# Optimization experiments

Hardware: AMD Instinct MI355X
Metric: run time of the kernel (lower is better)

## Reference

```python
import jax, jax.numpy as jnp
import numpy as np

DECAY = 0.97
TEMP = 0.7
EPS = 1e-6
NORM_EPS = 1e-12  # torch F.normalize default eps


def _l2norm(x, axis=-1):
    n = jnp.linalg.norm(x, axis=axis, keepdims=True)
    return x / jnp.maximum(n, NORM_EPS)


def setup_inputs() -> dict:
    key = jax.random.key(0)
    k1, k2, k3 = jax.random.split(key, 3)
    pair_embed = jax.random.normal(k1, (8, 2048, 1024), dtype=jnp.float32)
    patterns = _l2norm(jax.random.normal(k2, (4096, 1024), dtype=jnp.float32))
    usage = jax.random.uniform(k3, (4096,), dtype=jnp.float32)
    return {"pair_embed": pair_embed, "patterns": patterns, "usage": usage}


def reference(pair_embed, patterns, usage):
    G, D = patterns.shape
    flat = pair_embed.reshape(-1, D)                      # [N, D]
    queries = _l2norm(flat)
    pat_n = _l2norm(patterns)
    logits = queries @ pat_n.T                             # [N, G]
    homeostasis = jnp.log(jnp.clip(usage, EPS))
    weights = jax.nn.softmax((logits - homeostasis[None, :]) / TEMP, axis=-1)

    # Hebbian EMA update (mirrors update(); no_grad in original)
    flat_assign = weights                                  # [N, G]
    weights_sum = flat_assign.sum(axis=0)                  # [G]
    valid = weights_sum > 0
    usage_new = usage * DECAY
    usage_new = jnp.where(valid, usage_new + (1.0 - DECAY) * weights_sum, usage_new)
    updates = flat_assign.T @ flat                         # [G, D]
    updates = updates / (weights_sum[:, None] + EPS)
    blended = _l2norm(patterns * DECAY + (1.0 - DECAY) * updates)
    patterns_new = jnp.where(valid[:, None], blended, patterns)

    out_weights = weights.reshape(*pair_embed.shape[:-1], G)
    return out_weights, patterns_new, usage_new
```

## Files before the change

### kernel.cpp

```cpp
#include <hip/hip_runtime.h>
#include <stdint.h>
#include <math.h>


#define DECAY 0.97f
#define OMD 0.03f
#define INV_TEMP (1.0f / 0.7f)
#define EPS 1e-6f
#define NORM_EPS 1e-12f

constexpr int NROWS = 16384;
constexpr int DK = 1024;
constexpr int GP = 4096;

typedef unsigned short u16;
typedef __bf16 bf16x8 __attribute__((ext_vector_type(8)));
typedef float f32x4 __attribute__((ext_vector_type(4)));

__device__ inline u16 f2bf(float x) {
    union { float f; uint32_t u; } c; c.f = x;
    uint32_t r = c.u + 0x7fffu + ((c.u >> 16) & 1u);
    return (u16)(r >> 16);
}

__device__ inline void gl_lds16(const u16* g, u16* l) {
    __builtin_amdgcn_global_load_lds(
        (const __attribute__((address_space(1))) void*)g,
        (__attribute__((address_space(3))) void*)l, 16, 0, 0);
}

__global__ __launch_bounds__(256) void norm_rows_kernel(
        const float* __restrict__ in, u16* __restrict__ outn) {
    __shared__ float sred[4];
    const int row = blockIdx.x;
    const int t = threadIdx.x;
    const float4 v = ((const float4*)(in + (size_t)row * DK))[t];
    float ss = v.x * v.x + v.y * v.y + v.z * v.z + v.w * v.w;
#pragma unroll
    for (int o = 32; o > 0; o >>= 1) ss += __shfl_xor(ss, o);
    if ((t & 63) == 0) sred[t >> 6] = ss;
    __syncthreads();
    const float tot = sred[0] + sred[1] + sred[2] + sred[3];
    const float rs = 1.0f / fmaxf(sqrtf(tot), NORM_EPS);
    ushort4 o4;
    o4.x = f2bf(v.x * rs); o4.y = f2bf(v.y * rs);
    o4.z = f2bf(v.z * rs); o4.w = f2bf(v.w * rs);
    ((ushort4*)(outn + (size_t)row * DK))[t] = o4;
}

__global__ __launch_bounds__(256) void prep_scalars_kernel(
        const float* __restrict__ usage, float* __restrict__ hscaled,
        float* __restrict__ wsum, float* __restrict__ rowsum) {
    const int i = blockIdx.x * 256 + threadIdx.x;
    if (i < GP) {
        hscaled[i] = logf(fmaxf(usage[i], EPS)) * INV_TEMP;
        wsum[i] = 0.0f;
    }
    rowsum[i] = 0.0f;
}

__global__ __launch_bounds__(256) void rowinv_kernel(float* __restrict__ rowsum) {
    const int i = blockIdx.x * 256 + threadIdx.x;
    rowsum[i] = 1.0f / rowsum[i];
}

__global__ __launch_bounds__(256) void zero_kernel(float4* __restrict__ p) {
    p[(size_t)blockIdx.x * 256 + threadIdx.x] = (float4){0.f, 0.f, 0.f, 0.f};
}

__global__ __launch_bounds__(256) void transpose_f32_bf16_kernel(
        const float* __restrict__ in, u16* __restrict__ out, int R, int C) {
    __shared__ float tile[64][260];
    const int r0 = blockIdx.x * 64;
    const int c0 = blockIdx.y * 256;
    const int t = threadIdx.x;
    const int fr = t & 63;
    const int rr = t >> 6;
#pragma unroll
    for (int j = 0; j < 16; ++j) {
        const int r = rr + 4 * j;
        const float4 v = *(const float4*)(in + (size_t)(r0 + r) * C + c0 + fr * 4);
        *(float4*)&tile[r][fr * 4] = v;
    }
    __syncthreads();
    __align__(16) u16 tmp[64];
#pragma unroll
    for (int r = 0; r < 64; ++r) tmp[r] = f2bf(tile[r][t]);
    u16* op = out + (size_t)(c0 + t) * R + r0;
#pragma unroll
    for (int i = 0; i < 8; ++i) ((uint4*)op)[i] = ((const uint4*)tmp)[i];
}

__global__ __launch_bounds__(256) void scale_transpose_kernel(
        float* __restrict__ W, const float* __restrict__ invs,
        u16* __restrict__ wT, float* __restrict__ wsum) {
    __shared__ float tile[64][260];
    __shared__ float sinv[64];
    const int r0 = blockIdx.x * 64;
    const int c0 = blockIdx.y * 256;
    const int t = threadIdx.x;
    if (t < 64) sinv[t] = invs[r0 + t];
    __syncthreads();
    const int fr = t & 63;
    const int rr = t >> 6;
#pragma unroll
    for (int j = 0; j < 16; ++j) {
        const int r = rr + 4 * j;
        float4 v = *(const float4*)(W + (size_t)(r0 + r) * GP + c0 + fr * 4);
        const float s = sinv[r];
        v.x *= s; v.y *= s; v.z *= s; v.w *= s;
        *(float4*)(W + (size_t)(r0 + r) * GP + c0 + fr * 4) = v;
        *(float4*)&tile[r][fr * 4] = v;
    }
    __syncthreads();
    __align__(16) u16 tmp[64];
    float csum = 0.f;
#pragma unroll
    for (int r = 0; r < 64; ++r) {
        const float x = tile[r][t];
        csum += x;
        tmp[r] = f2bf(x);
    }
    u16* op = wT + (size_t)(c0 + t) * NROWS + r0;
#pragma unroll
    for (int i = 0; i < 8; ++i) ((uint4*)op)[i] = ((const uint4*)tmp)[i];
    atomicAdd(&wsum[c0 + t], csum);
}

template <int KSTEPS, int KLD>
__device__ inline void gemm_bt_tile(const u16* __restrict__ A,
                                    const u16* __restrict__ B,
                                    int m0, int n0, int k0,
                                    u16* As, u16* Bs, f32x4 acc[4][4]) {
    const int t = threadIdx.x;
    const int lane = t & 63;
    const int wave = t >> 6;
    const int wm = (wave >> 1) * 64;
    const int wn = (wave & 1) * 64;
    const int fr = lane & 15;
    const int q8 = lane >> 4;

    const int srow = 32 * wave + (lane >> 3);
    const int soct = (lane & 7) ^ ((lane >> 3) & 7);
    const size_t a_base = (size_t)(m0 + srow) * KLD + k0 + soct * 8;
    const size_t b_base = (size_t)(n0 + srow) * KLD + k0 + soct * 8;

#pragma unroll 1
    for (int kt = 0; kt < KSTEPS; kt += 64) {
        __syncthreads();
#pragma unroll
        for (int i = 0; i < 4; ++i) {
            gl_lds16(A + a_base + (size_t)(8 * i) * KLD + kt,
                     As + (32 * wave + 8 * i) * 64);
            gl_lds16(B + b_base + (size_t)(8 * i) * KLD + kt,
                     Bs + (32 * wave + 8 * i) * 64);
        }
        __syncthreads();
#pragma unroll
        for (int ks8 = 0; ks8 < 8; ks8 += 4) {
            bf16x8 af[4], bfr[4];
#pragma unroll
            for (int f = 0; f < 4; ++f) {
                const int ra = wm + f * 16 + fr;
                af[f]  = *(const bf16x8*)(As + ra * 64 + (((ks8 + q8) ^ (ra & 7)) * 8));
                const int rb = wn + f * 16 + fr;
                bfr[f] = *(const bf16x8*)(Bs + rb * 64 + (((ks8 + q8) ^ (rb & 7)) * 8));
            }
#pragma unroll
            for (int fm = 0; fm < 4; ++fm)
#pragma unroll
                for (int fn = 0; fn < 4; ++fn)
                    acc[fm][fn] = __builtin_amdgcn_mfma_f32_16x16x32_bf16(
                        af[fm], bfr[fn], acc[fm][fn], 0, 0, 0);
        }
    }
}

__global__ __launch_bounds__(256) void gemm1_kernel(
        const u16* __restrict__ Q, const u16* __restrict__ P,
        const float* __restrict__ hs, float* __restrict__ Wout,
        float* __restrict__ rowsum) {
    __shared__ u16 As[128 * 64];
    __shared__ u16 Bs[128 * 64];
    const int bid0 = blockIdx.x;
    const int bid = (bid0 & 7) * 512 + (bid0 >> 3);
    const int m0 = (bid >> 5) * 128;
    const int n0 = (bid & 31) * 128;
    f32x4 acc[4][4];
#pragma unroll
    for (int a = 0; a < 4; ++a)
#pragma unroll
        for (int b = 0; b < 4; ++b) acc[a][b] = (f32x4){0.f, 0.f, 0.f, 0.f};
    gemm_bt_tile<DK, DK>(Q, P, m0, n0, 0, As, Bs, acc);

    const int lane = threadIdx.x & 63;
    const int wave = threadIdx.x >> 6;
    const int wm = (wave >> 1) * 64, wn = (wave & 1) * 64;
    const int cq = lane & 15, rq = (lane >> 4) * 4;
    float hval[4];
#pragma unroll
    for (int fn = 0; fn < 4; ++fn) hval[fn] = hs[n0 + wn + fn * 16 + cq];
#pragma unroll
    for (int fm = 0; fm < 4; ++fm) {
        const int mb = m0 + wm + fm * 16 + rq;
#pragma unroll
        for (int r = 0; r < 4; ++r) {
            float rs = 0.f;
#pragma unroll
            for (int fn = 0; fn < 4; ++fn) {
                const int g = n0 + wn + fn * 16 + cq;
                const float e = __expf(acc[fm][fn][r] * INV_TEMP - hval[fn]);
                Wout[(size_t)(mb + r) * GP + g] = e;
                rs += e;
            }
#pragma unroll
            for (int o = 1; o < 16; o <<= 1) rs += __shfl_xor(rs, o);
            if (cq == 0) atomicAdd(&rowsum[mb + r], rs);
        }
    }
}

__global__ __launch_bounds__(256) void gemm2_kernel(
        const u16* __restrict__ WT, const u16* __restrict__ FT,
        float* __restrict__ Upart) {
    __shared__ u16 As[128 * 64];
    __shared__ u16 Bs[128 * 64];
    const int bid = blockIdx.x;
    const int k0 = (bid & 7) * 2048;
    const int n0 = ((bid >> 3) & 7) * 128;
    const int m0 = (bid >> 6) * 128;
    f32x4 acc[4][4];
#pragma unroll
    for (int a = 0; a < 4; ++a)
#pragma unroll
        for (int b = 0; b < 4; ++b) acc[a][b] = (f32x4){0.f, 0.f, 0.f, 0.f};
    gemm_bt_tile<2048, NROWS>(WT, FT, m0, n0, k0, As, Bs, acc);

    const int lane = threadIdx.x & 63;
    const int wave = threadIdx.x >> 6;
    const int wm = (wave >> 1) * 64, wn = (wave & 1) * 64;
    const int cq = lane & 15, rq = (lane >> 4) * 4;
#pragma unroll
    for (int fn = 0; fn < 4; ++fn) {
        const int d = n0 + wn + fn * 16 + cq;
#pragma unroll
        for (int fm = 0; fm < 4; ++fm) {
            const int gb = m0 + wm + fm * 16 + rq;
#pragma unroll
            for (int r = 0; r < 4; ++r)
                atomicAdd(&Upart[(size_t)(gb + r) * DK + d], acc[fm][fn][r]);
        }
    }
}

__global__ __launch_bounds__(256) void usage_kernel(
        const float* __restrict__ usage, const float* __restrict__ wsum,
        float* __restrict__ Uout, float* __restrict__ invw) {
    const int g = blockIdx.x * 256 + threadIdx.x;
    if (g < GP) {
        const float s = wsum[g];
        Uout[g] = usage[g] * DECAY + (s > 0.f ? OMD * s : 0.f);
        invw[g] = 1.0f / (s + EPS);
    }
}

__global__ __launch_bounds__(256) void finalize_patterns_kernel(
        const float* __restrict__ patterns, const float* __restrict__ wsum,
        const float* __restrict__ invw, const float* __restrict__ Upart,
        float* __restrict__ Pout) {
    __shared__ float sred[4];
    const int g = blockIdx.x;
    const int t = threadIdx.x;
    const float iw = invw[g] * OMD;
    const float4 u4 = ((const float4*)(Upart + (size_t)g * DK))[t];
    const float4 p4 = ((const float4*)(patterns + (size_t)g * DK))[t];
    float4 b;
    b.x = DECAY * p4.x + iw * u4.x;
    b.y = DECAY * p4.y + iw * u4.y;
    b.z = DECAY * p4.z + iw * u4.z;
    b.w = DECAY * p4.w + iw * u4.w;
    float ss = b.x * b.x + b.y * b.y + b.z * b.z + b.w * b.w;
#pragma unroll
    for (int o = 32; o > 0; o >>= 1) ss += __shfl_xor(ss, o);
    if ((t & 63) == 0) sred[t >> 6] = ss;
    __syncthreads();
    const float tot = sred[0] + sred[1] + sred[2] + sred[3];
    const float rs = 1.0f / fmaxf(sqrtf(tot), NORM_EPS);
    float4 o4;
    if (wsum[g] > 0.f) {
        o4.x = b.x * rs; o4.y = b.y * rs; o4.z = b.z * rs; o4.w = b.w * rs;
    } else {
        o4 = p4;
    }
    ((float4*)(Pout + (size_t)g * DK))[t] = o4;
}

extern "C" void kernel_launch(void* const* d_in, const int* in_sizes, int n_in,
                              void* d_out, int out_size, void* d_ws, size_t ws_size,
                              hipStream_t stream) {
    const float* pair_embed = (const float*)d_in[0];
    const float* patterns   = (const float*)d_in[1];
    const float* usage      = (const float*)d_in[2];

    float* out_w = (float*)d_out;
    float* out_p = out_w + (size_t)NROWS * GP;
    float* out_u = out_p + (size_t)GP * DK;

    char* ws = (char*)d_ws;
    u16* q_bf   = (u16*)(ws);
    float* Upart = (float*)(ws);
    u16* pat_bf = (u16*)(ws + 33554432);
    u16* fT     = (u16*)(ws + 41943040);
    u16* wT     = (u16*)(ws + 75497472);
    float* hs   = (float*)(ws + 209715200);
    float* wsum = (float*)(ws + 209715200 + 16384);
    float* invw = (float*)(ws + 209715200 + 32768);
    float* rsum = (float*)(ws + 209715200 + 49152);

    prep_scalars_kernel<<<64, 256, 0, stream>>>(usage, hs, wsum, rsum);
    norm_rows_kernel<<<NROWS, 256, 0, stream>>>(pair_embed, q_bf);
    norm_rows_kernel<<<GP, 256, 0, stream>>>(patterns, pat_bf);
    {
        dim3 g(NROWS / 64, DK / 256);
        transpose_f32_bf16_kernel<<<g, 256, 0, stream>>>(pair_embed, fT, NROWS, DK);
    }
    gemm1_kernel<<<(NROWS / 128) * (GP / 128), 256, 0, stream>>>(q_bf, pat_bf, hs, out_w, rsum);
    rowinv_kernel<<<64, 256, 0, stream>>>(rsum);
    {
        dim3 g(NROWS / 64, GP / 256);
        scale_transpose_kernel<<<g, 256, 0, stream>>>(out_w, rsum, wT, wsum);
    }
    usage_kernel<<<16, 256, 0, stream>>>(usage, wsum, out_u, invw);
    zero_kernel<<<(GP * DK / 4) / 256, 256, 0, stream>>>((float4*)Upart);
    gemm2_kernel<<<8 * (GP / 128) * (DK / 128), 256, 0, stream>>>(wT, fT, Upart);
    finalize_patterns_kernel<<<GP, 256, 0, stream>>>(patterns, wsum, invw, Upart, out_p);
}
```

Measured before the change: 925.9 us.

## Use 256x128 tiles with 8 waves and triple-buffered LDS prefetch in GEMMs

Both GEMM kernels move from 128x128 tiles with 4 waves and a load-sync-compute loop to 256x128 tiles with 8 waves. A three-slot LDS ring prefetches two k-steps ahead using vmcnt waits and a single barrier per step. MFMA sections are raised to higher priority with setprio. The goal is to hide global-to-LDS latency and raise B-tile reuse, at the cost of about 144KB of LDS per block, which limits occupancy. The bid swizzle in gemm1 is also removed.

```diff
diff --git a/kernel.cpp b/kernel.cpp
--- a/kernel.cpp
+++ b/kernel.cpp
@@ -128,10 +128,12 @@
 }
 
 template <int KSTEPS, int KLD>
-__device__ inline void gemm_bt_tile(const u16* __restrict__ A,
-                                    const u16* __restrict__ B,
-                                    int m0, int n0, int k0,
-                                    u16* As, u16* Bs, f32x4 acc[4][4]) {
+__device__ inline void gemm_bt_256x128(const u16* __restrict__ A,
+                                       const u16* __restrict__ B,
+                                       int m0, int n0, int k0,
+                                       u16* sm, f32x4 acc[4][4]) {
+    constexpr int SLOT = 24576;
+    constexpr int BOFF = 16384;
     const int t = threadIdx.x;
     const int lane = t & 63;
     const int wave = t >> 6;
@@ -140,58 +142,85 @@
     const int fr = lane & 15;
     const int q8 = lane >> 4;
 
-    const int srow = 32 * wave + (lane >> 3);
-    const int soct = (lane & 7) ^ ((lane >> 3) & 7);
-    const size_t a_base = (size_t)(m0 + srow) * KLD + k0 + soct * 8;
-    const size_t b_base = (size_t)(n0 + srow) * KLD + k0 + soct * 8;
-
+    const int arow = 32 * wave + (lane >> 3);
+    const int brow = 16 * wave + (lane >> 3);
+    const size_t a_base = (size_t)(m0 + arow) * KLD + k0 + (((lane & 7) ^ (arow & 7)) * 8);
+    const size_t b_base = (size_t)(n0 + brow) * KLD + k0 + (((lane & 7) ^ (brow & 7)) * 8);
+
+    auto STAGE = [&](int slot, int kt) {
+        u16* sa = sm + slot * SLOT;
+        u16* sb = sa + BOFF;
+#pragma unroll
+        for (int i = 0; i < 4; ++i)
+            gl_lds16(A + a_base + (size_t)(8 * i) * KLD + kt,
+                     sa + (32 * wave + 8 * i) * 64);
+#pragma unroll
+        for (int i = 0; i < 2; ++i)
+            gl_lds16(B + b_base + (size_t)(8 * i) * KLD + kt,
+                     sb + (16 * wave + 8 * i) * 64);
+    };
+
+    STAGE(0, 0);
+    STAGE(1, 64);
+    asm volatile("s_waitcnt vmcnt(6)" ::: "memory");
+    __builtin_amdgcn_sched_barrier(0);
+    __builtin_amdgcn_s_barrier();
+    __builtin_amdgcn_sched_barrier(0);
+
+    int slot = 0;
 #pragma unroll 1
     for (int kt = 0; kt < KSTEPS; kt += 64) {
-        __syncthreads();
-#pragma unroll
-        for (int i = 0; i < 4; ++i) {
-            gl_lds16(A + a_base + (size_t)(8 * i) * KLD + kt,
-                     As + (32 * wave + 8 * i) * 64);
-            gl_lds16(B + b_base + (size_t)(8 * i) * KLD + kt,
-                     Bs + (32 * wave + 8 * i) * 64);
-        }
-        __syncthreads();
+        if (kt + 128 < KSTEPS) {
+            int ss = slot + 2; if (ss >= 3) ss -= 3;
+            STAGE(ss, kt + 128);
+        }
+        const u16* sa = sm + slot * SLOT;
+        const u16* sb = sa + BOFF;
 #pragma unroll
         for (int ks8 = 0; ks8 < 8; ks8 += 4) {
             bf16x8 af[4], bfr[4];
 #pragma unroll
             for (int f = 0; f < 4; ++f) {
                 const int ra = wm + f * 16 + fr;
-                af[f]  = *(const bf16x8*)(As + ra * 64 + (((ks8 + q8) ^ (ra & 7)) * 8));
+                af[f]  = *(const bf16x8*)(sa + ra * 64 + (((ks8 + q8) ^ (ra & 7)) * 8));
                 const int rb = wn + f * 16 + fr;
-                bfr[f] = *(const bf16x8*)(Bs + rb * 64 + (((ks8 + q8) ^ (rb & 7)) * 8));
+                bfr[f] = *(const bf16x8*)(sb + rb * 64 + (((ks8 + q8) ^ (rb & 7)) * 8));
             }
+            __builtin_amdgcn_s_setprio(1);
 #pragma unroll
             for (int fm = 0; fm < 4; ++fm)
 #pragma unroll
                 for (int fn = 0; fn < 4; ++fn)
                     acc[fm][fn] = __builtin_amdgcn_mfma_f32_16x16x32_bf16(
                         af[fm], bfr[fn], acc[fm][fn], 0, 0, 0);
-        }
-    }
-}
-
-__global__ __launch_bounds__(256) void gemm1_kernel(
+            __builtin_amdgcn_s_setprio(0);
+        }
+        if (kt + 128 < KSTEPS) {
+            asm volatile("s_waitcnt vmcnt(6)" ::: "memory");
+        } else if (kt + 64 < KSTEPS) {
+            asm volatile("s_waitcnt vmcnt(0)" ::: "memory");
+        }
+        __builtin_amdgcn_sched_barrier(0);
+        __builtin_amdgcn_s_barrier();
+        __builtin_amdgcn_sched_barrier(0);
+        slot = slot + 1; if (slot >= 3) slot -= 3;
+    }
+}
+
+__global__ __launch_bounds__(512) void gemm1_kernel(
         const u16* __restrict__ Q, const u16* __restrict__ P,
         const float* __restrict__ hs, float* __restrict__ Wout,
         float* __restrict__ rowsum) {
-    __shared__ u16 As[128 * 64];
-    __shared__ u16 Bs[128 * 64];
-    const int bid0 = blockIdx.x;
-    const int bid = (bid0 & 7) * 512 + (bid0 >> 3);
-    const int m0 = (bid >> 5) * 128;
+    __shared__ u16 sm[3 * 24576];
+    const int bid = blockIdx.x;
+    const int m0 = (bid >> 5) * 256;
     const int n0 = (bid & 31) * 128;
     f32x4 acc[4][4];
 #pragma unroll
     for (int a = 0; a < 4; ++a)
 #pragma unroll
         for (int b = 0; b < 4; ++b) acc[a][b] = (f32x4){0.f, 0.f, 0.f, 0.f};
-    gemm_bt_tile<DK, DK>(Q, P, m0, n0, 0, As, Bs, acc);
+    gemm_bt_256x128<DK, DK>(Q, P, m0, n0, 0, sm, acc);
 
     const int lane = threadIdx.x & 63;
     const int wave = threadIdx.x >> 6;
@@ -220,21 +249,20 @@
     }
 }
 
-__global__ __launch_bounds__(256) void gemm2_kernel(
+__global__ __launch_bounds__(512) void gemm2_kernel(
         const u16* __restrict__ WT, const u16* __restrict__ FT,
         float* __restrict__ Upart) {
-    __shared__ u16 As[128 * 64];
-    __shared__ u16 Bs[128 * 64];
+    __shared__ u16 sm[3 * 24576];
     const int bid = blockIdx.x;
     const int k0 = (bid & 7) * 2048;
     const int n0 = ((bid >> 3) & 7) * 128;
-    const int m0 = (bid >> 6) * 128;
+    const int m0 = (bid >> 6) * 256;
     f32x4 acc[4][4];
 #pragma unroll
     for (int a = 0; a < 4; ++a)
 #pragma unroll
         for (int b = 0; b < 4; ++b) acc[a][b] = (f32x4){0.f, 0.f, 0.f, 0.f};
-    gemm_bt_tile<2048, NROWS>(WT, FT, m0, n0, k0, As, Bs, acc);
+    gemm_bt_256x128<2048, NROWS>(WT, FT, m0, n0, k0, sm, acc);
 
     const int lane = threadIdx.x & 63;
     const int wave = threadIdx.x >> 6;
@@ -324,7 +352,7 @@
         dim3 g(NROWS / 64, DK / 256);
         transpose_f32_bf16_kernel<<<g, 256, 0, stream>>>(pair_embed, fT, NROWS, DK);
     }
-    gemm1_kernel<<<(NROWS / 128) * (GP / 128), 256, 0, stream>>>(q_bf, pat_bf, hs, out_w, rsum);
+    gemm1_kernel<<<(NROWS / 256) * (GP / 128), 512, 0, stream>>>(q_bf, pat_bf, hs, out_w, rsum);
     rowinv_kernel<<<64, 256, 0, stream>>>(rsum);
     {
         dim3 g(NROWS / 64, GP / 256);
@@ -332,6 +360,6 @@
     }
     usage_kernel<<<16, 256, 0, stream>>>(usage, wsum, out_u, invw);
     zero_kernel<<<(GP * DK / 4) / 256, 256, 0, stream>>>((float4*)Upart);
-    gemm2_kernel<<<8 * (GP / 128) * (DK / 128), 256, 0, stream>>>(wT, fT, Upart);
+    gemm2_kernel<<<8 * (GP / 256) * (DK / 128), 512, 0, stream>>>(wT, fT, Upart);
     finalize_patterns_kernel<<<GP, 256, 0, stream>>>(patterns, wsum, invw, Upart, out_p);
 }
```

New measurement: 894.5 us. 3.4% less time.
